# Optimization experiments

Hardware: AMD Instinct MI355X
Metric: run time of the kernel (lower is better)

The kernel has to match this reference:

```python
import jax, jax.numpy as jnp
import numpy as np

B_, L, D_MODEL = 8, 2048, 512
EXPAND, D_STATE, HEADDIM, NGROUPS, D_CONV = 2, 16, 64, 1, 4
D_INNER = EXPAND * D_MODEL            # 1024
NHEADS = D_INNER // HEADDIM           # 16
CONV_DIM = D_INNER + 2 * NGROUPS * D_STATE   # 1056
D_IN_PROJ = 2 * D_INNER + 2 * NGROUPS * D_STATE + NHEADS  # 2096
EPS = 1e-5


def _mamba_params(key):
    ks = jax.random.split(key, 5)
    in_proj_w = jax.random.normal(ks[0], (D_IN_PROJ, D_MODEL), jnp.float32) * (D_MODEL ** -0.5)
    conv_w = jax.random.normal(ks[1], (CONV_DIM, 1, D_CONV), jnp.float32) * (D_CONV ** -0.5)
    conv_b = jnp.zeros((CONV_DIM,), jnp.float32)
    # inverse-softplus of dt ~ U[1e-3, 0.1] (mamba-ssm style init)
    dt_bias = jnp.log(jnp.expm1(jax.random.uniform(ks[2], (NHEADS,), jnp.float32, 1e-3, 0.1)))
    A_log = jnp.log(jax.random.uniform(ks[3], (NHEADS,), jnp.float32, 1.0, 16.0))
    Dp = jnp.ones((NHEADS,), jnp.float32)
    norm_w = jnp.ones((D_INNER,), jnp.float32)
    out_proj_w = jax.random.normal(ks[4], (D_MODEL, D_INNER), jnp.float32) * (D_INNER ** -0.5)
    return [in_proj_w, conv_w, conv_b, dt_bias, A_log, Dp, norm_w, out_proj_w]


def setup_inputs() -> dict:
    key = jax.random.key(0)
    k0, k1, k2 = jax.random.split(key, 3)
    d = {"x": jax.random.normal(k0, (B_, L, D_MODEL), jnp.float32)}
    names = ["in_proj_w", "conv_w", "conv_b", "dt_bias", "A_log", "Dp", "norm_w", "out_proj_w"]
    for pre, k in (("fwd_", k1), ("bwd_", k2)):
        for n, p in zip(names, _mamba_params(k)):
            d[pre + n] = p
    return d


def _silu(v):
    return v * jax.nn.sigmoid(v)


def _mamba2(u, in_proj_w, conv_w, conv_b, dt_bias, A_log, Dp, norm_w, out_proj_w):
    b, l, _ = u.shape
    zxbcdt = u @ in_proj_w.T                                # (b,l,D_IN_PROJ)
    z, xBC, dt = jnp.split(zxbcdt, [D_INNER, D_INNER + CONV_DIM], axis=-1)
    # causal depthwise conv1d + silu
    xc = jnp.transpose(xBC, (0, 2, 1))                      # (b,C,l)
    xc = jax.lax.conv_general_dilated(xc, conv_w, (1,), [(D_CONV - 1, 0)],
                                      feature_group_count=CONV_DIM)
    xBC = _silu(jnp.transpose(xc, (0, 2, 1)) + conv_b)      # (b,l,C)
    xs, Bm, Cm = jnp.split(xBC, [D_INNER, D_INNER + NGROUPS * D_STATE], axis=-1)
    xs = xs.reshape(b, l, NHEADS, HEADDIM)
    Bm = Bm.reshape(b, l, NGROUPS, D_STATE)[:, :, 0]        # ngroups=1 -> (b,l,N)
    Cm = Cm.reshape(b, l, NGROUPS, D_STATE)[:, :, 0]
    dt = jax.nn.softplus(dt + dt_bias)                      # (b,l,H)
    A = -jnp.exp(A_log)                                     # (H,)
    dA = jnp.exp(dt * A)                                    # (b,l,H), in (0,1)

    def step(h, inp):
        dA_t, dt_t, x_t, B_t, C_t = inp
        h = h * dA_t[:, :, None, None] + jnp.einsum('bh,bhp,bn->bhpn', dt_t, x_t, B_t)
        y = jnp.einsum('bhpn,bn->bhp', h, C_t)
        return h, y

    h0 = jnp.zeros((b, NHEADS, HEADDIM, D_STATE), u.dtype)
    seq = (jnp.moveaxis(dA, 1, 0), jnp.moveaxis(dt, 1, 0), jnp.moveaxis(xs, 1, 0),
           jnp.moveaxis(Bm, 1, 0), jnp.moveaxis(Cm, 1, 0))
    _, ys = jax.lax.scan(step, h0, seq)
    y = jnp.moveaxis(ys, 0, 1) + xs * Dp[None, None, :, None]   # (b,l,H,P)
    y = y.reshape(b, l, D_INNER)
    # RMSNormGated (norm_before_gate=False): rmsnorm(y * silu(z)) * w
    y = y * _silu(z)
    y = y * jax.lax.rsqrt(jnp.mean(y * y, axis=-1, keepdims=True) + EPS) * norm_w
    return y @ out_proj_w.T


def reference(x,
              fwd_in_proj_w, fwd_conv_w, fwd_conv_b, fwd_dt_bias, fwd_A_log, fwd_Dp, fwd_norm_w, fwd_out_proj_w,
              bwd_in_proj_w, bwd_conv_w, bwd_conv_b, bwd_dt_bias, bwd_A_log, bwd_Dp, bwd_norm_w, bwd_out_proj_w):
    fwd = _mamba2(x, fwd_in_proj_w, fwd_conv_w, fwd_conv_b, fwd_dt_bias, fwd_A_log, fwd_Dp, fwd_norm_w, fwd_out_proj_w)
    bwd = _mamba2(x[:, ::-1], bwd_in_proj_w, bwd_conv_w, bwd_conv_b, bwd_dt_bias, bwd_A_log, bwd_Dp, bwd_norm_w, bwd_out_proj_w)
    return fwd + bwd[:, ::-1]
```

## Files before the change

kernel.cpp:

```cpp
#include <hip/hip_runtime.h>
#include <stdint.h>

#define L_SEQ   2048
#define BATCH   8
#define DMODEL  512
#define DINNER  1024
#define NHEADS  16
#define HEADDIM 64
#define DSTATE  16
#define CONVDIM 1056
#define DINPROJ 2096
#define NPROJ   4192
#define NPROJ_P 4224
#define NROWS   (BATCH*L_SEQ)
#define NCH     16
#define CHLEN   128
#define XBCW    1072

typedef __attribute__((ext_vector_type(8))) short short8;
typedef __attribute__((ext_vector_type(4))) float f32x4;

static __device__ __forceinline__ unsigned short f2bf(float f) {
    unsigned int u = __float_as_uint(f);
    u += 0x7FFF + ((u >> 16) & 1);
    return (unsigned short)(u >> 16);
}
static __device__ __forceinline__ float bf2f(unsigned short u) {
    return __uint_as_float((unsigned int)u << 16);
}
static __device__ __forceinline__ float silu(float v) {
    return v / (1.f + __expf(-v));
}
static __device__ __forceinline__ void glds16(const unsigned short* g, unsigned short* l) {
    __builtin_amdgcn_global_load_lds(
        (const __attribute__((address_space(1))) unsigned int*)g,
        (__attribute__((address_space(3))) unsigned int*)l, 16, 0, 0);
}

#define PREP_N1 (NROWS*DMODEL)
#define PREP_N2 (NPROJ_P*DMODEL)
#define PREP_N3 (512*2048)
__global__ void k_prep(const float* __restrict__ x,
                       const float* __restrict__ fwi, const float* __restrict__ bwi,
                       const float* __restrict__ fow, const float* __restrict__ bow,
                       unsigned short* __restrict__ XB, unsigned short* __restrict__ W1,
                       unsigned short* __restrict__ W2) {
    int i = blockIdx.x * 256 + threadIdx.x;
    if (i < PREP_N1) {
        XB[i] = f2bf(x[i]);
    } else if (i < PREP_N1 + PREP_N2) {
        int j = i - PREP_N1;
        const int FS = DINPROJ * DMODEL;
        W1[j] = (j < 2 * FS) ? f2bf(j < FS ? fwi[j] : bwi[j - FS]) : 0;
    } else if (i < PREP_N1 + PREP_N2 + PREP_N3) {
        int j = i - PREP_N1 - PREP_N2;
        int n = j >> 11, k = j & 2047;
        float v = (k < DINNER) ? fow[n * DINNER + k] : bow[n * DINNER + k - DINNER];
        W2[j] = f2bf(v);
    }
}

#define BM 64
#define BN 128
#define BK 32

#define GEMM_BODY(NROUNDS, EPILOGUE)                                                        \
    __shared__ __align__(16) unsigned short as[2][BM][BK];                                  \
    __shared__ __align__(16) unsigned short bs[2][BN][BK];                                  \
    const int tid = threadIdx.x;                                                            \
    const int lane = tid & 63;                                                              \
    const int wave = tid >> 6;                                                              \
    const int wm = (wave & 1) * 32;                                                         \
    const int wn = (wave >> 1) * 64;                                                        \
    const int l16 = lane & 15;                                                              \
    const int q = lane >> 4;                                                                \
    const int sra = wave * 16;                                                              \
    const int srb = wave * 32;                                                              \
    const int lr = lane >> 2;                                                               \
    const int lc = (lane & 3) * 8;                                                          \
    f32x4 acc[2][4];                                                                        \
    for (int i = 0; i < 2; i++)                                                             \
        for (int j = 0; j < 4; j++) acc[i][j] = (f32x4){0.f, 0.f, 0.f, 0.f};                \
    const unsigned short* Ab = A + (size_t)(bm + sra + lr) * K + koff + lc;                 \
    const unsigned short* Bb = Bw + (size_t)(bn + srb + lr) * K + koff + lc;                \
    glds16(Ab, &as[0][sra][0]);                                                             \
    glds16(Bb, &bs[0][srb][0]);                                                             \
    glds16(Bb + (size_t)16 * K, &bs[0][srb + 16][0]);                                       \
    __syncthreads();                                                                        \
    for (int r = 0; r < NROUNDS; r++) {                                                     \
        const int pb = r & 1;                                                               \
        if (r + 1 < NROUNDS) {               \
            const int kb = (r + 1) * BK;                                                    \
            glds16(Ab + kb, &as[pb ^ 1][sra][0]);                                           \
            glds16(Bb + kb, &bs[pb ^ 1][srb][0]);                                           \
            glds16(Bb + (size_t)16 * K + kb, &bs[pb ^ 1][srb + 16][0]);                     \
        }                                                                                   \
        short8 af[2], bfr[4];                                                               \
        for (int i = 0; i < 2; i++) af[i] = *(const short8*)&as[pb][wm + i * 16 + l16][q * 8]; \
        for (int j = 0; j < 4; j++) bfr[j] = *(const short8*)&bs[pb][wn + j * 16 + l16][q * 8]; \
        for (int i = 0; i < 2; i++)                                                         \
            for (int j = 0; j < 4; j++)                                                     \
                acc[i][j] = __builtin_amdgcn_mfma_f32_16x16x32_bf16(af[i], bfr[j], acc[i][j], 0, 0, 0); \
        __syncthreads();            \
    }                                                                                       \
    EPILOGUE

__global__ __launch_bounds__(256) void k_gemm_proj(const unsigned short* __restrict__ A,
                                                   const unsigned short* __restrict__ Bw,
                                                   unsigned short* __restrict__ ZG,
                                                   unsigned short* __restrict__ XBCDT) {
    const int K = DMODEL;
    const int N = NPROJ;
    const int lin = blockIdx.x;
    const int xcd = lin & 7;
    const int idx = lin >> 3;
    const int mloc = idx & 31;
    const int n_tile = idx >> 5;
    const int bm = (mloc * 8 + xcd) * BM;
    const int bn = n_tile * BN;
    const int koff = 0;
    GEMM_BODY(16, {
        for (int i = 0; i < 2; i++) {
            int row0 = bm + wm + i * 16 + q * 4;
            for (int j = 0; j < 4; j++) {
                int col = bn + wn + j * 16 + l16;
                if (col < N) {
                    int dir = col >= DINPROJ;
                    int cc = col - dir * DINPROJ;
                    for (int r = 0; r < 4; r++) {
                        unsigned short v = f2bf(acc[i][j][r]);
                        size_t rowo = (size_t)(dir * NROWS + row0 + r);
                        if (cc < DINNER)
                            ZG[rowo * DINNER + cc] = v;
                        else
                            XBCDT[rowo * XBCW + (cc - DINNER)] = v;
                    }
                }
            }
        }
    })
}

__global__ __launch_bounds__(256) void k_gemm_out(const unsigned short* __restrict__ A,
                                                  const unsigned short* __restrict__ Bw,
                                                  float* __restrict__ C) {
    const int K = 2048;
    const int lin = blockIdx.x;
    const int xcd = lin & 7;
    const int idx = lin >> 3;
    const int mloc = idx & 31;
    const int n_tile = idx >> 5;
    const int bm = (mloc * 8 + xcd) * BM;
    const int bn = n_tile * BN;
    const int koff = 0;
    GEMM_BODY(64, {
        for (int i = 0; i < 2; i++) {
            int row0 = bm + wm + i * 16 + q * 4;
            for (int j = 0; j < 4; j++) {
                int col = bn + wn + j * 16 + l16;
                for (int r = 0; r < 4; r++)
                    C[(size_t)(row0 + r) * 512 + col] = acc[i][j][r];
            }
        }
    })
}

__global__ __launch_bounds__(256) void k_conv2(const unsigned short* __restrict__ XBCDT,
                                               const float* __restrict__ fw_w, const float* __restrict__ fw_b,
                                               const float* __restrict__ bw_w, const float* __restrict__ bw_b,
                                               unsigned short* __restrict__ XS, float* __restrict__ BCb) {
    __shared__ unsigned short sm[70][256];
    int t = threadIdx.x;
    int bidx = blockIdx.x;
    int lcn = bidx & 31;
    int b   = (bidx >> 5) & 7;
    int dir = (bidx >> 8) & 1;
    int ct  = bidx >> 9;
    int c0 = ct * 256;
    int l0 = lcn * 64;
    int c = c0 + t;
    const unsigned short* src = XBCDT + (size_t)dir * NROWS * XBCW;
    bool cok = (c < CONVDIM);
#pragma unroll 2
    for (int r = 0; r < 70; r++) {
        int li = l0 - 3 + r;
        unsigned short v = 0;
        if (li >= 0 && li < L_SEQ && cok)
            v = src[(size_t)((b << 11) + li) * XBCW + c];
        sm[r][t] = v;
    }
    __syncthreads();
    if (!cok) return;
    const float* w = (dir ? bw_w : fw_w) + c * 4;
    float bias = (dir ? bw_b : fw_b)[c];
    float wr[4];
    if (dir) { wr[0] = w[3]; wr[1] = w[2]; wr[2] = w[1]; wr[3] = w[0]; }
    else     { wr[0] = w[0]; wr[1] = w[1]; wr[2] = w[2]; wr[3] = w[3]; }
    int o = dir ? 3 : 0;
    float w0 = bf2f(sm[o][t]), w1 = bf2f(sm[o + 1][t]), w2 = bf2f(sm[o + 2][t]);
    unsigned short* xso = XS + (size_t)dir * NROWS * DINNER;
    float* bco = BCb + (size_t)dir * NROWS * 32;
    int rowbase = (b << 11) + l0;
#pragma unroll 4
    for (int l = 0; l < 64; l++) {
        float w3 = bf2f(sm[l + o + 3][t]);
        float acc = ((wr[0] * w0 + wr[1] * w1) + (wr[2] * w2 + wr[3] * w3)) + bias;
        float v = silu(acc);
        int row = rowbase + l;
        if (c < DINNER)
            xso[(size_t)row * DINNER + c] = f2bf(v);
        else
            bco[(size_t)row * 32 + (c - DINNER)] = v;
        w0 = w1; w1 = w2; w2 = w3;
    }
}

__global__ void k_dt(const unsigned short* __restrict__ XBCDT,
                     const float* __restrict__ fdtb, const float* __restrict__ fAl,
                     const float* __restrict__ bdtb, const float* __restrict__ bAl,
                     float* __restrict__ DT, float* __restrict__ DA) {
    int gid = blockIdx.x * 256 + threadIdx.x;
    if (gid >= 2 * NROWS * NHEADS) return;
    int h = gid & 15;
    int row = (gid >> 4) & (NROWS - 1);
    int dir = gid >> 18;
    float dtb = (dir ? bdtb : fdtb)[h];
    float Al = (dir ? bAl : fAl)[h];
    float x = bf2f(XBCDT[(size_t)(dir * NROWS + row) * XBCW + CONVDIM + h]) + dtb;
    float dt = (x > 15.f) ? x : log1pf(__expf(x));
    float dA = __expf(-__expf(Al) * dt);
    DT[gid] = dt;
    DA[gid] = dA;
}

__global__ __launch_bounds__(64) void k_scan_state(const unsigned short* __restrict__ XS,
                                                   const float* __restrict__ BCb,
                                                   const float* __restrict__ DT,
                                                   const float* __restrict__ DA,
                                                   float* __restrict__ S, float* __restrict__ P) {
    int idx = blockIdx.x;
    int c = idx & 15, h = (idx >> 4) & 15, b = (idx >> 8) & 7, dir = idx >> 11;
    int p = threadIdx.x;
    const unsigned short* xs = XS + (size_t)dir * NROWS * DINNER;
    const float* bc = BCb + (size_t)dir * NROWS * 32;
    const float* dtp = DT + (size_t)dir * NROWS * NHEADS;
    const float* dap = DA + (size_t)dir * NROWS * NHEADS;
    float hreg[16];
#pragma unroll
    for (int n = 0; n < 16; n++) hreg[n] = 0.f;
    float Pp = 1.f;
#pragma unroll 4
    for (int tl = 0; tl < CHLEN; ++tl) {
        int t = c * CHLEN + tl;
        int l = dir ? (L_SEQ - 1 - t) : t;
        int row = (b << 11) + l;
        float xv = bf2f(xs[(size_t)row * DINNER + h * HEADDIM + p]);
        float dt = dtp[row * 16 + h];
        float dA = dap[row * 16 + h];
        f32x4 Bv[4];
#pragma unroll
        for (int qq = 0; qq < 4; qq++) Bv[qq] = *(const f32x4*)&bc[(size_t)row * 32 + qq * 4];
        float kk = dt * xv;
#pragma unroll
        for (int n = 0; n < 16; n++) hreg[n] = fmaf(hreg[n], dA, kk * Bv[n >> 2][n & 3]);
        Pp *= dA;
    }
#pragma unroll
    for (int qq = 0; qq < 4; qq++) {
        f32x4 v = {hreg[qq * 4], hreg[qq * 4 + 1], hreg[qq * 4 + 2], hreg[qq * 4 + 3]};
        *(f32x4*)&S[(size_t)idx * 1024 + p * 16 + qq * 4] = v;
    }
    if (p == 0) P[idx] = Pp;
}

__global__ void k_combine(float* __restrict__ S, const float* __restrict__ P) {
    int gid = blockIdx.x * 256 + threadIdx.x;
    if (gid >= 2 * 8 * 16 * 1024) return;
    int pn = gid & 1023;
    int base = gid >> 10;
    float H = 0.f;
#pragma unroll 4
    for (int c = 0; c < NCH; c++) {
        size_t o = ((size_t)base * NCH + c) * 1024 + pn;
        float s = S[o];
        S[o] = H;
        H = H * P[base * NCH + c] + s;
    }
}

__global__ __launch_bounds__(64) void k_scan_out(const unsigned short* __restrict__ XS,
                                                 const float* __restrict__ BCb,
                                                 const float* __restrict__ DT,
                                                 const float* __restrict__ DA,
                                                 const float* __restrict__ Hinit,
                                                 const float* __restrict__ fDp,
                                                 const float* __restrict__ bDp,
                                                 unsigned short* __restrict__ Y) {
    int idx = blockIdx.x;
    int c = idx & 15, h = (idx >> 4) & 15, b = (idx >> 8) & 7, dir = idx >> 11;
    int p = threadIdx.x;
    const unsigned short* xs = XS + (size_t)dir * NROWS * DINNER;
    const float* bc = BCb + (size_t)dir * NROWS * 32;
    const float* dtp = DT + (size_t)dir * NROWS * NHEADS;
    const float* dap = DA + (size_t)dir * NROWS * NHEADS;
    unsigned short* yo = Y + (size_t)dir * NROWS * DINNER;
    float Dpv = (dir ? bDp : fDp)[h];
    float hreg[16];
#pragma unroll
    for (int qq = 0; qq < 4; qq++) {
        f32x4 v = *(const f32x4*)&Hinit[(size_t)idx * 1024 + p * 16 + qq * 4];
#pragma unroll
        for (int e = 0; e < 4; e++) hreg[qq * 4 + e] = v[e];
    }
#pragma unroll 4
    for (int tl = 0; tl < CHLEN; ++tl) {
        int t = c * CHLEN + tl;
        int l = dir ? (L_SEQ - 1 - t) : t;
        int row = (b << 11) + l;
        float xv = bf2f(xs[(size_t)row * DINNER + h * HEADDIM + p]);
        float dt = dtp[row * 16 + h];
        float dA = dap[row * 16 + h];
        f32x4 Bv[4], Cv[4];
#pragma unroll
        for (int qq = 0; qq < 4; qq++) Bv[qq] = *(const f32x4*)&bc[(size_t)row * 32 + qq * 4];
#pragma unroll
        for (int qq = 0; qq < 4; qq++) Cv[qq] = *(const f32x4*)&bc[(size_t)row * 32 + 16 + qq * 4];
        float kk = dt * xv;
        float y = 0.f;
#pragma unroll
        for (int n = 0; n < 16; n++) {
            hreg[n] = fmaf(hreg[n], dA, kk * Bv[n >> 2][n & 3]);
            y = fmaf(hreg[n], Cv[n >> 2][n & 3], y);
        }
        yo[(size_t)row * DINNER + h * HEADDIM + p] = f2bf(y + xv * Dpv);
    }
}

__global__ __launch_bounds__(256) void k_gatenorm(const unsigned short* __restrict__ Y,
                                                  const unsigned short* __restrict__ ZG,
                                                  const float* __restrict__ fnw,
                                                  const float* __restrict__ bnw,
                                                  unsigned short* __restrict__ NRM) {
    int bid = blockIdx.x;
    int t = threadIdx.x;
    int sub = t >> 7;
    int tt = t & 127;
    int rid = bid * 2 + sub;
    int dir = rid >> 14;
    int row = rid & (NROWS - 1);
    int c = tt * 8;
    const size_t base = (size_t)(dir * NROWS + row) * DINNER + c;
    uint4 yu = *(const uint4*)&Y[base];
    uint4 zu = *(const uint4*)&ZG[base];
    float v[8];
    {
        const unsigned int yw[4] = {yu.x, yu.y, yu.z, yu.w};
        const unsigned int zw[4] = {zu.x, zu.y, zu.z, zu.w};
#pragma unroll
        for (int e = 0; e < 4; e++) {
            v[e * 2]     = bf2f((unsigned short)(yw[e] & 0xffff)) * silu(bf2f((unsigned short)(zw[e] & 0xffff)));
            v[e * 2 + 1] = bf2f((unsigned short)(yw[e] >> 16))    * silu(bf2f((unsigned short)(zw[e] >> 16)));
        }
    }
    float ss = 0.f;
#pragma unroll
    for (int e = 0; e < 8; e++) ss += v[e] * v[e];
#pragma unroll
    for (int off = 32; off > 0; off >>= 1) ss += __shfl_down(ss, off);
    __shared__ float red[4];
    if ((t & 63) == 0) red[t >> 6] = ss;
    __syncthreads();
    float tot = red[sub * 2] + red[sub * 2 + 1];
    float scale = rsqrtf(tot * (1.f / 1024.f) + 1e-5f);
    const float* nw = (dir ? bnw : fnw) + c;
    f32x4 nw0 = *(const f32x4*)&nw[0];
    f32x4 nw1 = *(const f32x4*)&nw[4];
    unsigned int ow[4];
#pragma unroll
    for (int e = 0; e < 4; e++) {
        float a = v[e * 2]     * scale * (e < 2 ? nw0[e * 2]     : nw1[(e - 2) * 2]);
        float b = v[e * 2 + 1] * scale * (e < 2 ? nw0[e * 2 + 1] : nw1[(e - 2) * 2 + 1]);
        ow[e] = (unsigned int)f2bf(a) | ((unsigned int)f2bf(b) << 16);
    }
    uint4 o = {ow[0], ow[1], ow[2], ow[3]};
    *(uint4*)&NRM[(size_t)row * 2048 + dir * DINNER + c] = o;
}

extern "C" void kernel_launch(void* const* d_in, const int* in_sizes, int n_in,
                              void* d_out, int out_size, void* d_ws, size_t ws_size,
                              hipStream_t stream) {
    const float* x     = (const float*)d_in[0];
    const float* f_inw = (const float*)d_in[1];
    const float* f_cw  = (const float*)d_in[2];
    const float* f_cb  = (const float*)d_in[3];
    const float* f_dtb = (const float*)d_in[4];
    const float* f_Al  = (const float*)d_in[5];
    const float* f_Dp  = (const float*)d_in[6];
    const float* f_nw  = (const float*)d_in[7];
    const float* f_ow  = (const float*)d_in[8];
    const float* b_inw = (const float*)d_in[9];
    const float* b_cw  = (const float*)d_in[10];
    const float* b_cb  = (const float*)d_in[11];
    const float* b_dtb = (const float*)d_in[12];
    const float* b_Al  = (const float*)d_in[13];
    const float* b_Dp  = (const float*)d_in[14];
    const float* b_nw  = (const float*)d_in[15];
    const float* b_ow  = (const float*)d_in[16];

    char* ws = (char*)d_ws;
    size_t off = 0;
    auto alloc = [&](size_t bytes) {
        void* p = ws + off;
        off += (bytes + 255) & ~(size_t)255;
        return p;
    };
    unsigned short* XBCDT = (unsigned short*)alloc((size_t)2 * NROWS * XBCW * 2);
    unsigned short* NRM   = XBCDT;
    unsigned short* XS    = (unsigned short*)alloc((size_t)2 * NROWS * DINNER * 2);
    unsigned short* Yb    = XS;
    unsigned short* ZG    = (unsigned short*)alloc((size_t)2 * NROWS * DINNER * 2);
    unsigned short* W2    = (unsigned short*)alloc((size_t)512 * 2048 * 2);
    float* BCb  = (float*)alloc((size_t)2 * NROWS * 32 * 4);
    float* DT   = (float*)alloc((size_t)2 * NROWS * NHEADS * 4);
    float* DA   = (float*)alloc((size_t)2 * NROWS * NHEADS * 4);
    char* unionBase = (char*)alloc((size_t)16777216 + (size_t)NPROJ_P * DMODEL * 2);
    unsigned short* XB = (unsigned short*)unionBase;
    unsigned short* W1 = (unsigned short*)(unionBase + 16777216);
    float* S = (float*)unionBase;
    float* P = (float*)(unionBase + 16777216);

    if (ws_size < off) return;

    {
        int n = PREP_N1 + PREP_N2 + PREP_N3;
        k_prep<<<(n + 255) / 256, 256, 0, stream>>>(x, f_inw, b_inw, f_ow, b_ow, XB, W1, W2);
    }
    k_gemm_proj<<<8 * 32 * 33, 256, 0, stream>>>(XB, W1, ZG, XBCDT);
    k_conv2<<<5 * 2 * 8 * 32, 256, 0, stream>>>(XBCDT, f_cw, f_cb, b_cw, b_cb, XS, BCb);
    {
        int n = 2 * NROWS * NHEADS;
        k_dt<<<(n + 255) / 256, 256, 0, stream>>>(XBCDT, f_dtb, f_Al, b_dtb, b_Al, DT, DA);
    }
    k_scan_state<<<2 * 8 * 16 * NCH, 64, 0, stream>>>(XS, BCb, DT, DA, S, P);
    {
        int n = 2 * 8 * 16 * 1024;
        k_combine<<<(n + 255) / 256, 256, 0, stream>>>(S, P);
    }
    k_scan_out<<<2 * 8 * 16 * NCH, 64, 0, stream>>>(XS, BCb, DT, DA, S, f_Dp, b_Dp, Yb);
    k_gatenorm<<<NROWS, 256, 0, stream>>>(Yb, ZG, f_nw, b_nw, NRM);
    k_gemm_out<<<8 * 32 * 4, 256, 0, stream>>>(NRM, W2, (float*)d_out);
}
```

Measured before the change: 551.1 us.

## Enlarge GEMM tiles to 128x128x64 with swizzled LDS and split-K out-projection

The shared GEMM body now uses 128x128 tiles with BK=64 and a single LDS buffer. Each wave computes a 64x64 sub-tile, and an XOR swizzle on the LDS column groups is meant to avoid bank conflicts. The output projection splits K in two, writes the second half into the free ZG buffer, and a new elementwise kernel adds the partials. This raises data reuse per tile and keeps enough blocks for the smaller out GEMM. The cost is losing the double-buffer overlap between load and compute, plus an extra launch and an extra read/write pass over the output.

```diff
diff --git a/kernel.cpp b/kernel.cpp
--- a/kernel.cpp
+++ b/kernel.cpp
@@ -60,48 +60,52 @@
     }
 }
 
-#define BM 64
+#define BM 128
 #define BN 128
-#define BK 32
+#define BK 64
 
 #define GEMM_BODY(NROUNDS, EPILOGUE)                                                        \
-    __shared__ __align__(16) unsigned short as[2][BM][BK];                                  \
-    __shared__ __align__(16) unsigned short bs[2][BN][BK];                                  \
+    __shared__ __align__(16) unsigned short as[BM][BK];                                     \
+    __shared__ __align__(16) unsigned short bs[BN][BK];                                     \
     const int tid = threadIdx.x;                                                            \
     const int lane = tid & 63;                                                              \
     const int wave = tid >> 6;                                                              \
-    const int wm = (wave & 1) * 32;                                                         \
+    const int wm = (wave & 1) * 64;                                                         \
     const int wn = (wave >> 1) * 64;                                                        \
     const int l16 = lane & 15;                                                              \
     const int q = lane >> 4;                                                                \
-    const int sra = wave * 16;                                                              \
-    const int srb = wave * 32;                                                              \
-    const int lr = lane >> 2;                                                               \
-    const int lc = (lane & 3) * 8;                                                          \
-    f32x4 acc[2][4];                                                                        \
-    for (int i = 0; i < 2; i++)                                                             \
+    const int srow = wave * 8 + (lane >> 3);                                                \
+    const int sg = ((lane & 7) ^ (srow & 7)) * 8;                                           \
+    const int swz = l16 & 7;                                                                \
+    f32x4 acc[4][4];                                                                        \
+    for (int i = 0; i < 4; i++)                                                             \
         for (int j = 0; j < 4; j++) acc[i][j] = (f32x4){0.f, 0.f, 0.f, 0.f};                \
-    const unsigned short* Ab = A + (size_t)(bm + sra + lr) * K + koff + lc;                 \
-    const unsigned short* Bb = Bw + (size_t)(bn + srb + lr) * K + koff + lc;                \
-    glds16(Ab, &as[0][sra][0]);                                                             \
-    glds16(Bb, &bs[0][srb][0]);                                                             \
-    glds16(Bb + (size_t)16 * K, &bs[0][srb + 16][0]);                                       \
-    __syncthreads();                                                                        \
+    const unsigned short* Ab = A + (size_t)(bm + srow) * K + koff + sg;                     \
+    const unsigned short* Bb = Bw + (size_t)(bn + srow) * K + koff + sg;                    \
+    unsigned short* la = &as[wave * 8][0];                                                  \
+    unsigned short* lb = &bs[wave * 8][0];                                                  \
     for (int r = 0; r < NROUNDS; r++) {                                                     \
-        const int pb = r & 1;                                                               \
-        if (r + 1 < NROUNDS) {               \
-            const int kb = (r + 1) * BK;                                                    \
-            glds16(Ab + kb, &as[pb ^ 1][sra][0]);                                           \
-            glds16(Bb + kb, &bs[pb ^ 1][srb][0]);                                           \
-            glds16(Bb + (size_t)16 * K + kb, &bs[pb ^ 1][srb + 16][0]);                     \
+        const int kb = r * BK;                                                              \
+        glds16(Ab + kb, la);                                                                \
+        glds16(Ab + (size_t)32 * K + kb, la + 32 * BK);                                     \
+        glds16(Ab + (size_t)64 * K + kb, la + 64 * BK);                                     \
+        glds16(Ab + (size_t)96 * K + kb, la + 96 * BK);                                     \
+        glds16(Bb + kb, lb);                                                                \
+        glds16(Bb + (size_t)32 * K + kb, lb + 32 * BK);                                     \
+        glds16(Bb + (size_t)64 * K + kb, lb + 64 * BK);                                     \
+        glds16(Bb + (size_t)96 * K + kb, lb + 96 * BK);                                     \
+        __syncthreads();                                                                    \
+        for (int s = 0; s < 2; s++) {                                                      \
+            short8 af[4], bfr[4];                                                           \
+            for (int i = 0; i < 4; i++)                                                     \
+                af[i] = *(const short8*)&as[wm + i * 16 + l16][((s * 4 + q) ^ swz) * 8];    \
+            for (int j = 0; j < 4; j++)                                                     \
+                bfr[j] = *(const short8*)&bs[wn + j * 16 + l16][((s * 4 + q) ^ swz) * 8];   \
+            for (int i = 0; i < 4; i++)                                                     \
+                for (int j = 0; j < 4; j++)                                                 \
+                    acc[i][j] = __builtin_amdgcn_mfma_f32_16x16x32_bf16(af[i], bfr[j], acc[i][j], 0, 0, 0); \
         }                                                                                   \
-        short8 af[2], bfr[4];                                                               \
-        for (int i = 0; i < 2; i++) af[i] = *(const short8*)&as[pb][wm + i * 16 + l16][q * 8]; \
-        for (int j = 0; j < 4; j++) bfr[j] = *(const short8*)&bs[pb][wn + j * 16 + l16][q * 8]; \
-        for (int i = 0; i < 2; i++)                                                         \
-            for (int j = 0; j < 4; j++)                                                     \
-                acc[i][j] = __builtin_amdgcn_mfma_f32_16x16x32_bf16(af[i], bfr[j], acc[i][j], 0, 0, 0); \
-        __syncthreads();            \
+        __syncthreads();                                                                    \
     }                                                                                       \
     EPILOGUE
 
@@ -114,13 +118,13 @@
     const int lin = blockIdx.x;
     const int xcd = lin & 7;
     const int idx = lin >> 3;
-    const int mloc = idx & 31;
-    const int n_tile = idx >> 5;
+    const int mloc = idx & 15;
+    const int n_tile = idx >> 4;
     const int bm = (mloc * 8 + xcd) * BM;
     const int bn = n_tile * BN;
     const int koff = 0;
-    GEMM_BODY(16, {
-        for (int i = 0; i < 2; i++) {
+    GEMM_BODY(8, {
+        for (int i = 0; i < 4; i++) {
             int row0 = bm + wm + i * 16 + q * 4;
             for (int j = 0; j < 4; j++) {
                 int col = bn + wn + j * 16 + l16;
@@ -143,18 +147,24 @@
 
 __global__ __launch_bounds__(256) void k_gemm_out(const unsigned short* __restrict__ A,
                                                   const unsigned short* __restrict__ Bw,
-                                                  float* __restrict__ C) {
+                                                  float* __restrict__ C0,
+                                                  float* __restrict__ C1) {
     const int K = 2048;
     const int lin = blockIdx.x;
     const int xcd = lin & 7;
     const int idx = lin >> 3;
-    const int mloc = idx & 31;
-    const int n_tile = idx >> 5;
+    const int ksplit = idx >> 6;
+    const int rem = idx & 63;
+    const int g = rem >> 4;
+    const int r2 = rem & 15;
+    const int n_tile = r2 >> 2;
+    const int mloc = (g << 2) | (r2 & 3);
     const int bm = (mloc * 8 + xcd) * BM;
     const int bn = n_tile * BN;
-    const int koff = 0;
-    GEMM_BODY(64, {
-        for (int i = 0; i < 2; i++) {
+    const int koff = ksplit * 1024;
+    float* __restrict__ C = ksplit ? C1 : C0;
+    GEMM_BODY(16, {
+        for (int i = 0; i < 4; i++) {
             int row0 = bm + wm + i * 16 + q * 4;
             for (int j = 0; j < 4; j++) {
                 int col = bn + wn + j * 16 + l16;
@@ -163,6 +173,16 @@
             }
         }
     })
+}
+
+__global__ void k_addout(float* __restrict__ C0, const float* __restrict__ C1) {
+    int i = blockIdx.x * 256 + threadIdx.x;
+    if (i < NROWS * 512 / 4) {
+        f32x4 a = *(const f32x4*)&C0[i * 4];
+        f32x4 b = *(const f32x4*)&C1[i * 4];
+        a += b;
+        *(f32x4*)&C0[i * 4] = a;
+    }
 }
 
 __global__ __launch_bounds__(256) void k_conv2(const unsigned short* __restrict__ XBCDT,
@@ -419,6 +439,7 @@
     unsigned short* XS    = (unsigned short*)alloc((size_t)2 * NROWS * DINNER * 2);
     unsigned short* Yb    = XS;
     unsigned short* ZG    = (unsigned short*)alloc((size_t)2 * NROWS * DINNER * 2);
+    float* PBUF = (float*)ZG;
     unsigned short* W2    = (unsigned short*)alloc((size_t)512 * 2048 * 2);
     float* BCb  = (float*)alloc((size_t)2 * NROWS * 32 * 4);
     float* DT   = (float*)alloc((size_t)2 * NROWS * NHEADS * 4);
@@ -435,7 +456,7 @@
         int n = PREP_N1 + PREP_N2 + PREP_N3;
         k_prep<<<(n + 255) / 256, 256, 0, stream>>>(x, f_inw, b_inw, f_ow, b_ow, XB, W1, W2);
     }
-    k_gemm_proj<<<8 * 32 * 33, 256, 0, stream>>>(XB, W1, ZG, XBCDT);
+    k_gemm_proj<<<8 * 16 * 33, 256, 0, stream>>>(XB, W1, ZG, XBCDT);
     k_conv2<<<5 * 2 * 8 * 32, 256, 0, stream>>>(XBCDT, f_cw, f_cb, b_cw, b_cb, XS, BCb);
     {
         int n = 2 * NROWS * NHEADS;
@@ -448,5 +469,9 @@
     }
     k_scan_out<<<2 * 8 * 16 * NCH, 64, 0, stream>>>(XS, BCb, DT, DA, S, f_Dp, b_Dp, Yb);
     k_gatenorm<<<NROWS, 256, 0, stream>>>(Yb, ZG, f_nw, b_nw, NRM);
-    k_gemm_out<<<8 * 32 * 4, 256, 0, stream>>>(NRM, W2, (float*)d_out);
-}
+    k_gemm_out<<<8 * 128, 256, 0, stream>>>(NRM, W2, (float*)d_out, PBUF);
+    {
+        int n = NROWS * 512 / 4;
+        k_addout<<<(n + 255) / 256, 256, 0, stream>>>((float*)d_out, PBUF);
+    }
+}
```

New measurement: 578.7 us. 1.05x slower.
